# Performance work log

Measured on AMD Instinct MI355X. Metric: run time of the kernel, lower is better.

Reference implementation:

```python
import jax, jax.numpy as jnp
import numpy as np

B, T, D, F_FF, E, TOP_K = 8, 2048, 1024, 4096, 8, 2
CAP_FACTOR = 1.25


def setup_inputs() -> dict:
    key = jax.random.key(0)
    ks = jax.random.split(key, 7)
    s = 0.02
    return {
        "x": jax.random.normal(ks[0], (B, T, D), dtype=jnp.float32),
        "w_router": jax.random.normal(ks[1], (D, E), dtype=jnp.float32) * s,
        "b_router": jnp.zeros((E,), dtype=jnp.float32),
        "w1": jax.random.normal(ks[2], (E, D, F_FF), dtype=jnp.float32) * s,
        "b1": jnp.zeros((E, F_FF), dtype=jnp.float32),
        "w2": jax.random.normal(ks[3], (E, F_FF, D), dtype=jnp.float32) * s,
        "b2": jnp.zeros((E, D), dtype=jnp.float32),
    }


def reference(x, w_router, b_router, w1, b1, w2, b2):
    b, t, d = x.shape
    n = b * t
    e = w_router.shape[1]
    xf = x.reshape(n, d)

    # router in float32 (as original: .float())
    logits = xf.astype(jnp.float32) @ w_router + b_router
    gates = jax.nn.softmax(logits, axis=-1)              # [N, E]
    topv, topi = jax.lax.top_k(gates, TOP_K)             # [N, K]

    cap = max(1, int(CAP_FACTOR * n / e))

    # flatten assignments in (token, slot) order -> matches python loop order
    e_flat = topi.reshape(-1)                            # [N*K] expert id
    g_flat = topv.reshape(-1)                            # [N*K] gate value
    tok = jnp.repeat(jnp.arange(n), TOP_K)               # [N*K] token id

    # position of each assignment inside its expert (arrival order)
    onehot = jax.nn.one_hot(e_flat, e, dtype=jnp.int32)  # [N*K, E]
    pos = jnp.cumsum(onehot, axis=0)[jnp.arange(n * TOP_K), e_flat] - 1
    keep = pos < cap                                     # capacity dropping
    posc = jnp.minimum(pos, cap - 1)

    # dispatch: [E, cap, D] buffers (unique kept slots -> scatter-add safe)
    buf = jnp.zeros((e, cap, d), x.dtype).at[e_flat, posc].add(
        jnp.where(keep[:, None], xf[tok], 0.0))

    # per-expert FFN as grouped GEMM (exact GELU, as torch nn.GELU default)
    h = jax.nn.gelu(jnp.einsum('ecd,edf->ecf', buf, w1) + b1[:, None, :],
                    approximate=False)
    out = jnp.einsum('ecf,efd->ecd', h, w2) + b2[:, None, :]

    # combine: weighted scatter-add back to tokens
    og = out[e_flat, posc]                               # [N*K, D]
    w = jnp.where(keep, g_flat, 0.0).astype(x.dtype)
    y = jnp.zeros((n, d), x.dtype).at[tok].add(w[:, None] * og)
    ws = jnp.zeros((n,), x.dtype).at[tok].add(w)
    y = jnp.where((ws > 0.0)[:, None], y / jnp.maximum(ws, 1e-6)[:, None], y)
    return y.reshape(b, t, d)
```

## Files before the change

### kernel.cpp

```cpp
#include <hip/hip_runtime.h>

#define NTOK   16384
#define DMODEL 1024
#define FFF    4096
#define NEXP   8
#define CAP    2560
#define NASSIGN (NTOK*2)

typedef __bf16 bf16x8 __attribute__((ext_vector_type(8)));
typedef float  f32x4  __attribute__((ext_vector_type(4)));
typedef unsigned short u16x8 __attribute__((ext_vector_type(8)));

template<int V> struct IC { static constexpr int value = V; };

__device__ __forceinline__ unsigned short f2bf(float f) {
    unsigned int u = __float_as_uint(f);
    u = u + 0x7FFFu + ((u >> 16) & 1u);
    return (unsigned short)(u >> 16);
}
__device__ __forceinline__ float bf2f(unsigned short s) {
    return __uint_as_float(((unsigned int)s) << 16);
}

__device__ void router_body(int rb, const float* __restrict__ x,
                            const float* __restrict__ wr,
                            const float* __restrict__ br,
                            int* __restrict__ topi,
                            float* __restrict__ topv) {
    int t    = rb * 4 + (threadIdx.x >> 6);
    int lane = threadIdx.x & 63;
    const float4* xr4 = reinterpret_cast<const float4*>(x + (size_t)t * DMODEL);
    float a[8] = {0.f,0.f,0.f,0.f,0.f,0.f,0.f,0.f};
    #pragma unroll
    for (int i = lane; i < DMODEL/4; i += 64) {
        float4 xv = xr4[i];
        const float* w = wr + i * 32;
        #pragma unroll
        for (int e = 0; e < 8; e++) a[e] = fmaf(xv.x, w[e],      a[e]);
        #pragma unroll
        for (int e = 0; e < 8; e++) a[e] = fmaf(xv.y, w[8 + e],  a[e]);
        #pragma unroll
        for (int e = 0; e < 8; e++) a[e] = fmaf(xv.z, w[16 + e], a[e]);
        #pragma unroll
        for (int e = 0; e < 8; e++) a[e] = fmaf(xv.w, w[24 + e], a[e]);
    }
    #pragma unroll
    for (int off = 32; off > 0; off >>= 1) {
        #pragma unroll
        for (int e = 0; e < 8; e++) a[e] += __shfl_xor(a[e], off, 64);
    }
    if (lane == 0) {
        float l[8], g[8];
        float mx = -1e30f;
        #pragma unroll
        for (int e = 0; e < 8; e++) { l[e] = a[e] + br[e]; mx = fmaxf(mx, l[e]); }
        float s = 0.f;
        #pragma unroll
        for (int e = 0; e < 8; e++) { g[e] = expf(l[e] - mx); s += g[e]; }
        float inv = 1.f / s;
        #pragma unroll
        for (int e = 0; e < 8; e++) g[e] *= inv;
        float v1 = -1.f, v2 = -1.f; int i1 = 0, i2 = 0;
        #pragma unroll
        for (int e = 0; e < 8; e++) {
            float v = g[e];
            if (v > v1)      { v2 = v1; i2 = i1; v1 = v; i1 = e; }
            else if (v > v2) { v2 = v; i2 = e; }
        }
        topi[t*2]   = i1; topi[t*2+1] = i2;
        topv[t*2]   = v1; topv[t*2+1] = v2;
    }
}

__device__ void transpose_body(const float* __restrict__ src,
                               unsigned short* __restrict__ dst,
                               int R, int C, int r0, int c0) {
    __shared__ float tile[64 * 65];
    int t = threadIdx.x;
    int lr4 = (t & 15) * 4;
    #pragma unroll
    for (int s = 0; s < 4; s++) {
        int r = (t >> 4) + s * 16;
        float4 v = *reinterpret_cast<const float4*>(&src[(size_t)(r0 + r) * C + c0 + lr4]);
        float* tr = &tile[r * 65 + lr4];
        tr[0] = v.x; tr[1] = v.y; tr[2] = v.z; tr[3] = v.w;
    }
    __syncthreads();
    int j = t & 7;
    int ccb = t >> 3;
    #pragma unroll
    for (int s = 0; s < 2; s++) {
        int cc = ccb + s * 32;
        u16x8 o;
        #pragma unroll
        for (int k = 0; k < 8; k++) o[k] = f2bf(tile[(j * 8 + k) * 65 + cc]);
        *reinterpret_cast<u16x8*>(&dst[(size_t)(c0 + cc) * R + r0 + j * 8]) = o;
    }
}

__global__ void prologue_kernel(const float* __restrict__ x,
                                const float* __restrict__ wr,
                                const float* __restrict__ br,
                                const float* __restrict__ w1,
                                const float* __restrict__ w2,
                                int* __restrict__ topi,
                                float* __restrict__ topv,
                                unsigned short* __restrict__ w1t,
                                unsigned short* __restrict__ w2t) {
    int id = blockIdx.x;
    if (id < NTOK/4) {
        router_body(id, x, wr, br, topi, topv);
    } else if (id < NTOK/4 + 8192) {
        int q = id - NTOK/4;
        int e = q >> 10, t = q & 1023;
        int bx = t & 63, by = t >> 6;
        transpose_body(w1 + (size_t)e * DMODEL * FFF,
                       w1t + (size_t)e * DMODEL * FFF,
                       DMODEL, FFF, by * 64, bx * 64);
    } else {
        int q = id - NTOK/4 - 8192;
        int e = q >> 10, t = q & 1023;
        int bx = t & 15, by = t >> 4;
        transpose_body(w2 + (size_t)e * DMODEL * FFF,
                       w2t + (size_t)e * DMODEL * FFF,
                       FFF, DMODEL, by * 64, bx * 64);
    }
}

__global__ void scan_kernel(const int* __restrict__ topi,
                            int* __restrict__ pos,
                            int* __restrict__ slot_tok,
                            int* __restrict__ kept) {
    const int APT = NASSIGN / 256;
    int tid = threadIdx.x, lane = tid & 63, w = tid >> 6;
    int base = tid * APT;
    const int4* tp = reinterpret_cast<const int4*>(topi + base);
    int c[8] = {0,0,0,0,0,0,0,0};
    for (int i = 0; i < APT/4; i++) {
        int4 v = tp[i];
        #pragma unroll
        for (int q = 0; q < 8; q++)
            c[q] += (v.x == q) + (v.y == q) + (v.z == q) + (v.w == q);
    }
    int excl[8], wtot[8];
    #pragma unroll
    for (int e = 0; e < 8; e++) {
        int s = c[e];
        for (int off = 1; off < 64; off <<= 1) {
            int n = __shfl_up(s, off, 64);
            if (lane >= off) s += n;
        }
        excl[e] = s - c[e];
        wtot[e] = __shfl(s, 63, 64);
    }
    __shared__ int woff[4][8];
    if (lane == 0) {
        #pragma unroll
        for (int e = 0; e < 8; e++) woff[w][e] = wtot[e];
    }
    __syncthreads();
    if (tid == 0) {
        for (int e = 0; e < 8; e++) {
            int run = 0;
            for (int ww = 0; ww < 4; ww++) { int t0 = woff[ww][e]; woff[ww][e] = run; run += t0; }
            kept[e] = run < CAP ? run : CAP;
        }
    }
    __syncthreads();
    int run[8];
    #pragma unroll
    for (int e = 0; e < 8; e++) run[e] = woff[w][e] + excl[e];
    for (int i = 0; i < APT/4; i++) {
        int4 v = tp[i];
        int ev[4] = {v.x, v.y, v.z, v.w};
        #pragma unroll
        for (int u = 0; u < 4; u++) {
            int a = base + i*4 + u;
            int e = ev[u];
            int p = 0;
            #pragma unroll
            for (int q = 0; q < 8; q++) if (e == q) { p = run[q]; run[q] = p + 1; }
            pos[a] = p;
            if (p < CAP) slot_tok[(size_t)e * CAP + p] = a >> 1;
        }
    }
}

__global__ void dispatch_kernel(const float* __restrict__ x,
                                const int* __restrict__ slot_tok,
                                const int* __restrict__ kept,
                                unsigned short* __restrict__ xb) {
    int row  = blockIdx.x * 4 + (threadIdx.x >> 6);
    int lane = threadIdx.x & 63;
    int e = row / CAP;
    int p = row - e * CAP;
    if (p >= kept[e]) return;
    int t = slot_tok[row];
    const float4* src = reinterpret_cast<const float4*>(x + (size_t)t * DMODEL);
    ushort4* dst = reinterpret_cast<ushort4*>(xb + (size_t)row * DMODEL);
    #pragma unroll
    for (int i = lane; i < DMODEL/4; i += 64) {
        float4 v = src[i];
        ushort4 o;
        o.x = f2bf(v.x); o.y = f2bf(v.y); o.z = f2bf(v.z); o.w = f2bf(v.w);
        dst[i] = o;
    }
}

template<int GELU>
__global__ __launch_bounds__(512, 2)
void gemm_8p(const unsigned short* __restrict__ A,
             const unsigned short* __restrict__ Bt,
             const float* __restrict__ bias,
             unsigned short* __restrict__ C,
             int M, int N, int K) {
    constexpr int BM = 256, BN = 256, BK = 64;
    __shared__ __align__(16) unsigned short As[2][BM * BK];
    __shared__ __align__(16) unsigned short Bs[2][BN * BK];

    const int e = blockIdx.z;
    const int gx = N / BN, gy = M / BM;
    const int nc = gx < 8 ? gx : 8;
    int id = blockIdx.x;
    const int per_chunk = nc * gy;
    const int chunk = id / per_chunk;
    const int r = id - chunk * per_chunk;
    const int bn = chunk * nc + (r % nc);
    const int bm = r / nc;

    const unsigned short* Ab = A  + (size_t)e * M * K + (size_t)bm * BM * K;
    const unsigned short* Bb = Bt + (size_t)e * N * K + (size_t)bn * BN * K;
    const float* bp = bias + (size_t)e * N;

    const int tid  = threadIdx.x;
    const int lane = tid & 63;
    const int wv   = tid >> 6;
    const int half = wv >> 2;
    const int wn   = (wv & 3) * 64;
    const int lr   = lane & 15;
    const int quad = lane >> 4;

    const int ksx   = (quad ^ (lr & 7)) * 8;
    const int aoff0 = (half * 32 + lr) * 64 + ksx;
    const int boff0 = ((wv & 3) * 64 + lr) * 64 + ksx;
    const unsigned short* a00 = &As[0][aoff0];
    const unsigned short* a01 = &As[0][aoff0 ^ 32];
    const unsigned short* a10 = &As[1][aoff0];
    const unsigned short* a11 = &As[1][aoff0 ^ 32];
    const unsigned short* b00 = &Bs[0][boff0];
    const unsigned short* b01 = &Bs[0][boff0 ^ 32];
    const unsigned short* b10 = &Bs[1][boff0];
    const unsigned short* b11 = &Bs[1][boff0 ^ 32];

    const int sprow  = tid >> 3;
    const int schunk = (tid & 7) ^ (sprow & 7);
    const size_t K32 = (size_t)32 * K;
    const unsigned short* gA0 = Ab + (size_t)((sprow & 31) + ((sprow >> 5) << 7)) * K + schunk * 8;
    const unsigned short* gB0 = Bb + (size_t)sprow * K + schunk * 8;

    auto stageA = [&](int pb, int kt, int g) {
        __builtin_amdgcn_global_load_lds(
            (const __attribute__((address_space(1))) unsigned int*)
                (gA0 + (size_t)g * K32 + kt * BK),
            (__attribute__((address_space(3))) unsigned int*)
                (&As[pb][g * 4096 + wv * 512]),
            16, 0, 0);
    };
    auto stageB = [&](int pb, int kt, int h2) {
        __builtin_amdgcn_global_load_lds(
            (const __attribute__((address_space(1))) unsigned int*)
                (gB0 + (size_t)h2 * 2 * K32 + kt * BK),
            (__attribute__((address_space(3))) unsigned int*)
                (&Bs[pb][h2 * 4096 + wv * 512]),
            16, 0, 0);
    };

    f32x4 acc[8][4] = {};
    const int NT = K / BK;

    stageA(0, 0, 0); stageA(0, 0, 1); stageA(0, 0, 2); stageA(0, 0, 3);
    stageB(0, 0, 0); stageB(0, 0, 1); stageB(0, 0, 2); stageB(0, 0, 3);
    stageB(1, 1, 0); stageB(1, 1, 1); stageB(1, 1, 2); stageB(1, 1, 3);
    stageA(1, 1, 0); stageA(1, 1, 1);
    asm volatile("s_waitcnt vmcnt(6)" ::: "memory");
    __builtin_amdgcn_s_barrier();

    auto tile = [&](auto pc, int tt) {
        constexpr int P = decltype(pc)::value;
        const unsigned short* aK0 = P ? a10 : a00;
        const unsigned short* aK1 = P ? a11 : a01;
        const unsigned short* bK0 = P ? b10 : b00;
        const unsigned short* bK1 = P ? b11 : b01;
        bf16x8 bfr[4][2];
        #pragma unroll
        for (int q = 0; q < 4; ++q) {
            bf16x8 af[2][2];
            #pragma unroll
            for (int i2 = 0; i2 < 2; ++i2) {
                af[i2][0] = *reinterpret_cast<const bf16x8*>(aK0 + q * 4096 + i2 * 1024);
                af[i2][1] = *reinterpret_cast<const bf16x8*>(aK1 + q * 4096 + i2 * 1024);
            }
            if (q == 0) {
                #pragma unroll
                for (int jf = 0; jf < 4; ++jf) {
                    bfr[jf][0] = *reinterpret_cast<const bf16x8*>(bK0 + jf * 1024);
                    bfr[jf][1] = *reinterpret_cast<const bf16x8*>(bK1 + jf * 1024);
                }
            }
            if (q == 0)      { if (tt + 1 < NT) { stageA(P ^ 1, tt + 1, 2); stageA(P ^ 1, tt + 1, 3); } }
            else if (q == 1) { if (tt + 2 < NT) { stageB(P, tt + 2, 0); stageB(P, tt + 2, 1); } }
            else if (q == 2) { if (tt + 2 < NT) { stageB(P, tt + 2, 2); stageB(P, tt + 2, 3); } }
            else             { if (tt + 2 < NT) { stageA(P, tt + 2, 0); stageA(P, tt + 2, 1); } }

            __builtin_amdgcn_s_barrier();
            asm volatile("s_waitcnt lgkmcnt(0)" ::: "memory");
            __builtin_amdgcn_s_setprio(1);
            #pragma unroll
            for (int ks = 0; ks < 2; ++ks) {
                #pragma unroll
                for (int i2 = 0; i2 < 2; ++i2) {
                    #pragma unroll
                    for (int jf = 0; jf < 4; ++jf) {
                        acc[q * 2 + i2][jf] = __builtin_amdgcn_mfma_f32_16x16x32_bf16(
                            af[i2][ks], bfr[jf][ks], acc[q * 2 + i2][jf], 0, 0, 0);
                    }
                }
            }
            __builtin_amdgcn_s_setprio(0);
            if (q == 3) {
                if (tt + 2 < NT)      asm volatile("s_waitcnt vmcnt(6)" ::: "memory");
                else if (tt + 1 < NT) asm volatile("s_waitcnt vmcnt(0)" ::: "memory");
            }
            __builtin_amdgcn_s_barrier();
        }
    };

    for (int t = 0; t < NT; t += 2) {
        tile(IC<0>{}, t);
        tile(IC<1>{}, t + 1);
    }

    size_t cbase = (size_t)e * M * N + (size_t)bm * BM * N + (size_t)bn * BN;
    float bv[4];
    #pragma unroll
    for (int jf = 0; jf < 4; ++jf) bv[jf] = bp[bn * BN + wn + jf * 16 + lr];
    #pragma unroll
    for (int m = 0; m < 8; ++m) {
        #pragma unroll
        for (int rr = 0; rr < 4; ++rr) {
            int row = half * 128 + (m >> 1) * 32 + (m & 1) * 16 + quad * 4 + rr;
            #pragma unroll
            for (int jf = 0; jf < 4; ++jf) {
                int col = wn + jf * 16 + lr;
                float v = acc[m][jf][rr] + bv[jf];
                if (GELU) v = 0.5f * v * (1.f + erff(v * 0.70710678118654752440f));
                C[cbase + (size_t)row * N + col] = f2bf(v);
            }
        }
    }
}

__global__ void combine_kernel(const int* __restrict__ topi,
                               const float* __restrict__ topv,
                               const int* __restrict__ pos,
                               const unsigned short* __restrict__ out2,
                               float* __restrict__ y) {
    int t    = blockIdx.x * 4 + (threadIdx.x >> 6);
    int lane = threadIdx.x & 63;
    int e0 = topi[t*2],   e1 = topi[t*2+1];
    float g0 = topv[t*2], g1 = topv[t*2+1];
    int p0 = pos[t*2],    p1 = pos[t*2+1];
    float w0 = (p0 < CAP) ? g0 : 0.f;
    float w1 = (p1 < CAP) ? g1 : 0.f;
    float wsum = w0 + w1;
    float scale = (wsum > 0.f) ? 1.f / fmaxf(wsum, 1e-6f) : 0.f;
    int q0 = p0 < CAP ? p0 : CAP - 1;
    int q1 = p1 < CAP ? p1 : CAP - 1;
    const ushort4* o0 = reinterpret_cast<const ushort4*>(out2 + ((size_t)e0 * CAP + q0) * DMODEL);
    const ushort4* o1 = reinterpret_cast<const ushort4*>(out2 + ((size_t)e1 * CAP + q1) * DMODEL);
    float4* dst = reinterpret_cast<float4*>(y + (size_t)t * DMODEL);
    #pragma unroll
    for (int i = lane; i < DMODEL/4; i += 64) {
        ushort4 a = o0[i], b = o1[i];
        float4 r;
        r.x = (w0 * bf2f(a.x) + w1 * bf2f(b.x)) * scale;
        r.y = (w0 * bf2f(a.y) + w1 * bf2f(b.y)) * scale;
        r.z = (w0 * bf2f(a.z) + w1 * bf2f(b.z)) * scale;
        r.w = (w0 * bf2f(a.w) + w1 * bf2f(b.w)) * scale;
        dst[i] = r;
    }
}

extern "C" void kernel_launch(void* const* d_in, const int* in_sizes, int n_in,
                              void* d_out, int out_size, void* d_ws, size_t ws_size,
                              hipStream_t stream) {
    (void)in_sizes; (void)n_in; (void)out_size; (void)ws_size;
    const float* x        = (const float*)d_in[0];
    const float* w_router = (const float*)d_in[1];
    const float* b_router = (const float*)d_in[2];
    const float* w1       = (const float*)d_in[3];
    const float* b1       = (const float*)d_in[4];
    const float* w2       = (const float*)d_in[5];
    const float* b2       = (const float*)d_in[6];
    float* y = (float*)d_out;

    char* ws = (char*)d_ws;
    size_t off = 0;
    auto alloc = [&](size_t n) { char* p = ws + off; off = (off + n + 255) & ~(size_t)255; return p; };
    int*   topi     = (int*)  alloc((size_t)NASSIGN * 4);
    float* topv     = (float*)alloc((size_t)NASSIGN * 4);
    int*   pos      = (int*)  alloc((size_t)NASSIGN * 4);
    int*   slot_tok = (int*)  alloc((size_t)NEXP * CAP * 4);
    int*   kept     = (int*)  alloc(8 * 4);
    unsigned short* w1t = (unsigned short*)alloc((size_t)NEXP * DMODEL * FFF * 2);
    unsigned short* w2t = (unsigned short*)alloc((size_t)NEXP * DMODEL * FFF * 2);
    unsigned short* xb  = (unsigned short*)alloc((size_t)NEXP * CAP * DMODEL * 2);
    unsigned short* h   = (unsigned short*)alloc((size_t)NEXP * CAP * FFF * 2);
    unsigned short* out2 = w1t;

    prologue_kernel<<<NTOK/4 + 16384, 256, 0, stream>>>(
        x, w_router, b_router, w1, w2, topi, topv, w1t, w2t);
    scan_kernel<<<1, 256, 0, stream>>>(topi, pos, slot_tok, kept);
    dispatch_kernel<<<NEXP*CAP/4, 256, 0, stream>>>(x, slot_tok, kept, xb);
    gemm_8p<1><<<dim3((FFF/256)*(CAP/256), 1, NEXP), 512, 0, stream>>>(xb, w1t, b1, h, CAP, FFF, DMODEL);
    gemm_8p<0><<<dim3((DMODEL/256)*(CAP/256), 1, NEXP), 512, 0, stream>>>(h, w2t, b2, out2, CAP, DMODEL, FFF);
    combine_kernel<<<NTOK/4, 256, 0, stream>>>(topi, topv, pos, out2, y);
}
```

Baseline: 949.4 us.

## Use 128x128 GEMM kernel for second expert matmul and remap block tile order

Adds a new gemm_bt kernel with 128x128 tiles, 4 waves and single-buffered direct global-to-LDS loads, and uses it for the second FFN GEMM (K=4096, N=1024). At 256x256 tiles that GEMM has only 4x10 tiles per expert, so the smaller tiles raise the block count and improve CU occupancy. The 8-phase kernel's block-to-tile mapping is also changed to group blocks by M-chunks of 8 rows instead of N-chunks. The new kernel has no double buffering and synchronises twice per K step, which may expose memory latency, and the smaller tiles reduce operand reuse.

Result: no change. 946.3 us (-0.3%).

```diff
diff --git a/kernel.cpp b/kernel.cpp
--- a/kernel.cpp
+++ b/kernel.cpp
@@ -220,13 +220,14 @@
 
     const int e = blockIdx.z;
     const int gx = N / BN, gy = M / BM;
-    const int nc = gx < 8 ? gx : 8;
     int id = blockIdx.x;
-    const int per_chunk = nc * gy;
-    const int chunk = id / per_chunk;
-    const int r = id - chunk * per_chunk;
-    const int bn = chunk * nc + (r % nc);
-    const int bm = r / nc;
+    const int cw = 8 * gx;
+    const int chunk = id / cw;
+    const int rr0 = id - chunk * cw;
+    const int rem = gy - chunk * 8;
+    const int mcw = rem < 8 ? rem : 8;
+    const int bm = chunk * 8 + rr0 % mcw;
+    const int bn = rr0 / mcw;
 
     const unsigned short* Ab = A  + (size_t)e * M * K + (size_t)bm * BM * K;
     const unsigned short* Bb = Bt + (size_t)e * N * K + (size_t)bn * BN * K;
@@ -353,6 +354,96 @@
             for (int jf = 0; jf < 4; ++jf) {
                 int col = wn + jf * 16 + lr;
                 float v = acc[m][jf][rr] + bv[jf];
+                if (GELU) v = 0.5f * v * (1.f + erff(v * 0.70710678118654752440f));
+                C[cbase + (size_t)row * N + col] = f2bf(v);
+            }
+        }
+    }
+}
+
+template<int GELU>
+__global__ __launch_bounds__(256, 2)
+void gemm_bt(const unsigned short* __restrict__ A,
+             const unsigned short* __restrict__ Bt,
+             const float* __restrict__ bias,
+             unsigned short* __restrict__ C,
+             int M, int N, int K) {
+    constexpr int BM = 128, BN = 128, BK = 64;
+    __shared__ unsigned short As[BM * 64];
+    __shared__ unsigned short Bs[BN * 64];
+    const int e = blockIdx.z;
+    const int gx = N / BN, gy = M / BM;
+    const int nc = gx < 8 ? gx : 8;
+    int id = blockIdx.x;
+    const int per_chunk = nc * gy;
+    const int chunk = id / per_chunk;
+    const int r = id - chunk * per_chunk;
+    const int bn = chunk * nc + (r % nc);
+    const int bm = r / nc;
+
+    const unsigned short* Ab = A  + (size_t)e * M * K + (size_t)bm * BM * K;
+    const unsigned short* Bb = Bt + (size_t)e * N * K + (size_t)bn * BN * K;
+    const float* bp = bias + (size_t)e * N;
+    const int tid  = threadIdx.x;
+    const int lane = tid & 63;
+    const int wv   = tid >> 6;
+    const int wm   = (wv >> 1) * 64;
+    const int wn   = (wv & 1) * 64;
+    const int lr   = lane & 15;
+    const int quad = lane >> 4;
+    const int srow   = lane >> 3;
+    const int schunk = (lane & 7) ^ srow;
+    const int swiz   = lr & 7;
+
+    f32x4 acc[4][4] = {};
+
+    for (int kb = 0; kb < K; kb += BK) {
+        #pragma unroll
+        for (int s = 0; s < 4; s++) {
+            int q = wv * 4 + s;
+            int row = q * 8 + srow;
+            __builtin_amdgcn_global_load_lds(
+                (const __attribute__((address_space(1))) unsigned int*)(Ab + (size_t)row * K + kb + schunk * 8),
+                (__attribute__((address_space(3))) unsigned int*)(As + q * 512),
+                16, 0, 0);
+            __builtin_amdgcn_global_load_lds(
+                (const __attribute__((address_space(1))) unsigned int*)(Bb + (size_t)row * K + kb + schunk * 8),
+                (__attribute__((address_space(3))) unsigned int*)(Bs + q * 512),
+                16, 0, 0);
+        }
+        __syncthreads();
+        #pragma unroll
+        for (int kk = 0; kk < BK; kk += 32) {
+            bf16x8 af[4], bfr[4];
+            const int sc = ((kk >> 3) + quad) ^ swiz;
+            #pragma unroll
+            for (int i = 0; i < 4; i++)
+                af[i] = *reinterpret_cast<const bf16x8*>(&As[(wm + i*16 + lr) * 64 + sc * 8]);
+            #pragma unroll
+            for (int j = 0; j < 4; j++)
+                bfr[j] = *reinterpret_cast<const bf16x8*>(&Bs[(wn + j*16 + lr) * 64 + sc * 8]);
+            #pragma unroll
+            for (int i = 0; i < 4; i++)
+                #pragma unroll
+                for (int j = 0; j < 4; j++)
+                    acc[i][j] = __builtin_amdgcn_mfma_f32_16x16x32_bf16(af[i], bfr[j], acc[i][j], 0, 0, 0);
+        }
+        __syncthreads();
+    }
+
+    size_t cbase = (size_t)e * M * N + (size_t)bm * BM * N + (size_t)bn * BN;
+    float bv[4];
+    #pragma unroll
+    for (int j = 0; j < 4; j++) bv[j] = bp[bn * BN + wn + j * 16 + lr];
+    #pragma unroll
+    for (int i = 0; i < 4; i++) {
+        #pragma unroll
+        for (int rr = 0; rr < 4; rr++) {
+            int row = wm + i * 16 + quad * 4 + rr;
+            #pragma unroll
+            for (int j = 0; j < 4; j++) {
+                int col = wn + j * 16 + lr;
+                float v = acc[i][j][rr] + bv[j];
                 if (GELU) v = 0.5f * v * (1.f + erff(v * 0.70710678118654752440f));
                 C[cbase + (size_t)row * N + col] = f2bf(v);
             }
@@ -423,6 +514,6 @@
     scan_kernel<<<1, 256, 0, stream>>>(topi, pos, slot_tok, kept);
     dispatch_kernel<<<NEXP*CAP/4, 256, 0, stream>>>(x, slot_tok, kept, xb);
     gemm_8p<1><<<dim3((FFF/256)*(CAP/256), 1, NEXP), 512, 0, stream>>>(xb, w1t, b1, h, CAP, FFF, DMODEL);
-    gemm_8p<0><<<dim3((DMODEL/256)*(CAP/256), 1, NEXP), 512, 0, stream>>>(h, w2t, b2, out2, CAP, DMODEL, FFF);
+    gemm_bt<0><<<dim3((DMODEL/128)*(CAP/128), 1, NEXP), 256, 0, stream>>>(h, w2t, b2, out2, CAP, DMODEL, FFF);
     combine_kernel<<<NTOK/4, 256, 0, stream>>>(topi, topv, pos, out2, y);
 }
```
